# Optimization experiments

Measured on AMD Instinct MI355X. Metric: run time of the kernel, lower is better.

The kernel has to match this reference:

```python
import jax, jax.numpy as jnp
import numpy as np

N, E = 50000, 500000
DH, DL = 13, 128          # handcrafted / learned node feature dims
OH, OL = 32, 96           # node-encoder output dims; node_dim D = OH+OL
D = OH + OL               # 128
EIN = (DH + DL) + 1 + 3 * D + 1  # 527, forced by concat in forward
H = 256                   # MLP hidden width
HC = 64                   # classifier hidden width
EPS = 1e-8


def _mlp(x, W1, b1, W2, b2):
    # 2-layer MLP with ReLU, matching repo MLP(fc_dims=[H, out])
    return jax.nn.relu(x @ W1 + b1) @ W2 + b2


def _cosine(a, b):
    # torch.nn.CosineSimilarity(dim=1, eps=1e-8)
    na = jnp.maximum(jnp.linalg.norm(a, axis=-1), EPS)
    nb = jnp.maximum(jnp.linalg.norm(b, axis=-1), EPS)
    return jnp.sum(a * b, axis=-1) / (na * nb)


def _lin(key, fan_in, fan_out):
    kW, kb = jax.random.split(key)
    s = 1.0 / np.sqrt(fan_in)
    return (jax.random.uniform(kW, (fan_in, fan_out), jnp.float32, -s, s),
            jax.random.uniform(kb, (fan_out,), jnp.float32, -s, s))


def setup_inputs() -> dict:
    key = jax.random.key(0)
    ks = jax.random.split(key, 16)
    x1 = jax.random.normal(ks[0], (N, DH), jnp.float32)
    x2 = jax.random.normal(ks[1], (N, DL), jnp.float32)
    edge_index = jax.random.randint(ks[2], (2, E), 0, N, jnp.int64)
    Wh1, bh1 = _lin(ks[3], DH, H);   Wh2, bh2 = _lin(ks[4], H, OH)
    Wl1, bl1 = _lin(ks[5], DL, H);   Wl2, bl2 = _lin(ks[6], H, OL)
    We1, be1 = _lin(ks[7], EIN, H);  We2, be2 = _lin(ks[8], H, D)
    Wmsg, bmsg = _lin(ks[9], 2 * D, D)
    Wnode, bnode = _lin(ks[10], 2 * D, D)
    Wmp1, bmp1 = _lin(ks[11], 3 * D, H); Wmp2, bmp2 = _lin(ks[12], H, D)
    Wc1, bc1 = _lin(ks[13], D, HC);  Wc2, bc2 = _lin(ks[14], HC, 1)
    return dict(x1=x1, x2=x2, edge_index=edge_index,
                Wh1=Wh1, bh1=bh1, Wh2=Wh2, bh2=bh2,
                Wl1=Wl1, bl1=bl1, Wl2=Wl2, bl2=bl2,
                We1=We1, be1=be1, We2=We2, be2=be2,
                Wmsg=Wmsg, bmsg=bmsg, Wnode=Wnode, bnode=bnode,
                Wmp1=Wmp1, bmp1=bmp1, Wmp2=Wmp2, bmp2=bmp2,
                Wc1=Wc1, bc1=bc1, Wc2=Wc2, bc2=bc2)


def reference(x1, x2, edge_index,
              Wh1, bh1, Wh2, bh2,
              Wl1, bl1, Wl2, bl2,
              We1, be1, We2, be2,
              Wmsg, bmsg, Wnode, bnode,
              Wmp1, bmp1, Wmp2, bmp2,
              Wc1, bc1, Wc2, bc2):
    src, trg = edge_index[0], edge_index[1]
    # raw-feature edge descriptors
    x_init = jnp.concatenate((x1, x2), axis=-1)            # [N, 141]
    xi_s, xi_t = x_init[src], x_init[trg]                  # gathers [E, 141]
    sim1 = _cosine(xi_s, xi_t)                             # [E]
    abs_init = jnp.abs(xi_s - xi_t)                        # [E, 141]
    # node encoders
    h1 = _mlp(x1, Wh1, bh1, Wh2, bh2)                      # [N, 32]
    h2 = _mlp(x2, Wl1, bl1, Wl2, bl2)                      # [N, 96]
    x = jnp.concatenate((h1, h2), axis=-1)                 # [N, 128]
    xs, xt = x[src], x[trg]                                # [E, 128]
    sim2 = _cosine(xs, xt)                                 # [E]
    edge_feat_in = jnp.concatenate(
        (abs_init, sim1[:, None], xs, xt, jnp.abs(xs - xt), sim2[:, None]),
        axis=-1)                                           # [E, 527]
    e = _mlp(edge_feat_in, We1, be1, We2, be2)             # [E, 128]
    # edge MPNN round: edge->node aggregation, node update, edge update
    msg = jax.nn.relu(jnp.concatenate((xs, e), axis=-1) @ Wmsg + bmsg)  # [E, 128]
    agg = jax.ops.segment_sum(msg, trg, num_segments=N)    # [N, 128]
    xn = jax.nn.relu(jnp.concatenate((x, agg), axis=-1) @ Wnode + bnode)  # [N, 128]
    e_mp = _mlp(jnp.concatenate((xn[src], xn[trg], e), axis=-1),
                Wmp1, bmp1, Wmp2, bmp2)                    # [E, 128]
    pred = _mlp(e_mp, Wc1, bc1, Wc2, bc2)                  # [E, 1]
    return jnp.squeeze(pred, axis=-1)                      # [E]
```

## Files before the change

kernel.cpp:

```cpp
#include <hip/hip_runtime.h>
#include <hip/hip_bf16.h>
#include <hip/hip_fp16.h>


using fp16 = __half;
typedef _Float16 h16;
typedef _Float16 f16x8 __attribute__((ext_vector_type(8)));
typedef float f32x4 __attribute__((ext_vector_type(4)));

#define NN 50000
#define EE 500000
#define EPSC 1e-8f

__device__ __forceinline__ float reluf(float v){ return v > 0.f ? v : 0.f; }

#define OFF_E1   0
#define OFF_E2   139264
#define OFF_MSG  172032
#define OFF_NODE 204800
#define OFF_MP1  237568
#define OFF_MP2  335872
#define OFF_C1   368640
#define OFF_N1   376832
#define OFF_N2   458752
#define WT_TOTAL 524288
#define BF_TOTAL 640

__global__ __launch_bounds__(256) void k_prep(
    const float* __restrict__ We1, const float* __restrict__ We2,
    const float* __restrict__ Wmsg, const float* __restrict__ Wnode,
    const float* __restrict__ Wmp1, const float* __restrict__ Wmp2,
    const float* __restrict__ Wc1,
    const float* __restrict__ Wh1, const float* __restrict__ Wl1,
    const float* __restrict__ Wh2, const float* __restrict__ Wl2,
    const float* __restrict__ bh1, const float* __restrict__ bl1,
    const float* __restrict__ bh2, const float* __restrict__ bl2,
    h16* __restrict__ WT, float* __restrict__ BF)
{
  int idx = blockIdx.x * 256 + threadIdx.x;
  if (idx >= WT_TOTAL) {
    const int b = idx - WT_TOTAL;
    if (b < 512) BF[b] = (b < 256) ? bh1[b] : bl1[b - 256];
    else if (b < BF_TOTAL) {
      const int c = b - 512;
      BF[b] = (c < 32) ? bh2[c] : bl2[c - 32];
    }
    return;
  }
  h16 v;
  if (idx < OFF_E2) {
    const int L = idx, n = L / 544, k = L % 544;
    int r;
    if      (k < 128) r = 142 + k;
    else if (k < 256) r = 270 + (k - 128);
    else if (k < 384) r = 398 + (k - 256);
    else if (k < 512) r = 13 + (k - 384);
    else if (k < 525) r = k - 512;
    else if (k == 528) r = 141;
    else if (k == 529) r = 526;
    else r = -1;
    v = (h16)((r >= 0) ? We1[r * 256 + n] : 0.f);
  } else if (idx < OFF_MSG) {
    const int L = idx - OFF_E2, n = L >> 8, k = L & 255;
    v = (h16)We2[k * 128 + n];
  } else if (idx < OFF_NODE) {
    const int L = idx - OFF_MSG, n = L >> 8, k = L & 255;
    const int ko = (k < 128) ? (128 + k) : (k - 128);
    v = (h16)Wmsg[ko * 128 + n];
  } else if (idx < OFF_MP1) {
    const int L = idx - OFF_NODE, n = L >> 8, k = L & 255;
    v = (h16)Wnode[k * 128 + n];
  } else if (idx < OFF_MP2) {
    const int L = idx - OFF_MP1, n = L / 384, k = L % 384;
    v = (h16)Wmp1[k * 256 + n];
  } else if (idx < OFF_C1) {
    const int L = idx - OFF_MP2, n = L >> 8, k = L & 255;
    v = (h16)Wmp2[k * 128 + n];
  } else if (idx < OFF_N1) {
    const int L = idx - OFF_C1, n = L >> 7, k = L & 127;
    v = (h16)Wc1[k * 64 + n];
  } else if (idx < OFF_N2) {
    const int L = idx - OFF_N1, n = L / 160, k = L % 160;
    float f = 0.f;
    if (n < 256) { if (k < 13) f = Wh1[k * 256 + n]; }
    else { if (k >= 16 && k < 144) f = Wl1[(k - 16) * 256 + (n - 256)]; }
    v = (h16)f;
  } else {
    const int L = idx - OFF_N2, n = L >> 9, k = L & 511;
    float f = 0.f;
    if (n < 32) { if (k < 256) f = Wh2[k * 32 + n]; }
    else { if (k >= 256) f = Wl2[(k - 256) * 96 + (n - 32)]; }
    v = (h16)f;
  }
  WT[idx] = v;
}

__global__ __launch_bounds__(256) void k_cvt(
    const float* __restrict__ x1, const float* __restrict__ x2,
    h16* __restrict__ X1P, h16* __restrict__ X2H)
{
  const int idx = blockIdx.x * 256 + threadIdx.x;
  if (idx < NN * 16) {
    const int nn = idx >> 4, j = idx & 15;
    X1P[idx] = (h16)((j < 13) ? x1[nn * 13 + j] : 0.f);
  }
  const int i2 = idx - NN * 16;
  if (i2 >= 0 && i2 < NN * 128) X2H[i2] = (h16)x2[i2];
}

template<int ROWS, int UDIM, int KP, int LDA, int WAVES, bool RELU,
         bool ENDSYNC, typename F>
__device__ __forceinline__ void mfma_gemm(const h16* sA,
    const h16* __restrict__ WT, const float* __restrict__ bias, F emit)
{
  constexpr int RT = ROWS / 16;
  constexpr int NPW0 = UDIM / WAVES;
  constexpr int NPW = (NPW0 < 16) ? 16 : NPW0;
  constexpr int NT = NPW / 16;
  constexpr int NSTEPS = KP / 32;
  constexpr int CH0 = (NT >= 4) ? 2 : 4;
  constexpr int CHUNK = (NSTEPS < CH0) ? NSTEPS : CH0;
  constexpr int NCH = (NSTEPS + CHUNK - 1) / CHUNK;
  const int tid = threadIdx.x;
  const int wave = tid >> 6;
  const int lane = tid & 63;
  const int m = lane & 15;
  const int quad = lane >> 4;
  const int n0 = wave * NPW;
  const bool active = (n0 < UDIM);

  f32x4 acc[RT][NT];
#pragma unroll
  for (int r = 0; r < RT; ++r)
#pragma unroll
    for (int j = 0; j < NT; ++j) acc[r][j] = (f32x4){0.f, 0.f, 0.f, 0.f};
  float bb[NT];

  if (active) {
    const h16* wbase = &WT[(size_t)(n0 + m) * KP + quad * 8];
#pragma unroll
    for (int j = 0; j < NT; ++j) bb[j] = bias[n0 + j * 16 + m];

    f16x8 breg[2][CHUNK][NT];
#pragma unroll
    for (int s = 0; s < CHUNK; ++s)
      if (s < NSTEPS)
#pragma unroll
        for (int j = 0; j < NT; ++j)
          breg[0][s][j] = *(const f16x8*)&wbase[(size_t)j * 16 * KP + s * 32];
    asm volatile("" ::: "memory");

#pragma unroll
    for (int c = 0; c < NCH; ++c) {
      if (c + 1 < NCH) {
#pragma unroll
        for (int s = 0; s < CHUNK; ++s) {
          const int st = (c + 1) * CHUNK + s;
          if (st < NSTEPS)
#pragma unroll
            for (int j = 0; j < NT; ++j)
              breg[(c + 1) & 1][s][j] =
                  *(const f16x8*)&wbase[(size_t)j * 16 * KP + st * 32];
        }
      }
#pragma unroll
      for (int s = 0; s < CHUNK; ++s) {
        const int st = c * CHUNK + s;
        if (st < NSTEPS) {
          const int k0 = st * 32;
#pragma unroll
          for (int r = 0; r < RT; ++r) {
            const f16x8 af = *(const f16x8*)&sA[(r * 16 + m) * LDA + k0 + quad * 8];
#pragma unroll
            for (int j = 0; j < NT; ++j)
              acc[r][j] = __builtin_amdgcn_mfma_f32_16x16x32_f16(af, breg[c & 1][s][j], acc[r][j], 0, 0, 0);
          }
        }
      }
      asm volatile("" ::: "memory");
    }
  }
  __syncthreads();
  if (active) {
#pragma unroll
    for (int j = 0; j < NT; ++j) {
      const int col = n0 + j * 16 + m;
#pragma unroll
      for (int r = 0; r < RT; ++r)
#pragma unroll
        for (int g = 0; g < 4; ++g) {
          const int row = r * 16 + quad * 4 + g;
          float v = acc[r][j][g] + bb[j];
          if (RELU) v = reluf(v);
          emit(row, col, v);
        }
    }
  }
  if (ENDSYNC) __syncthreads();
}

__global__ __launch_bounds__(512, 4) void k_nenc(
    const h16* __restrict__ X1P, const h16* __restrict__ X2H,
    const h16* __restrict__ WT, const float* __restrict__ BF,
    h16* __restrict__ XH)
{
  __shared__ __align__(16) h16 sA[32 * 168];
  __shared__ __align__(16) h16 sH[32 * 520];
  const int tid = threadIdx.x;
  const int n0 = blockIdx.x * 32;
  const int remn = NN - n0;
  const int cnt = remn < 32 ? remn : 32;
  const int n = tid >> 4;
  const int q = tid & 15;

  if (n < cnt) {
    const int node = n0 + n;
    if (q < 2)
      *(f16x8*)&sA[n * 168 + q * 8] = *(const f16x8*)&X1P[node * 16 + q * 8];
    else if (q < 4)
      *(f16x8*)&sA[n * 168 + 144 + (q - 2) * 8] = (f16x8){};
    *(f16x8*)&sA[n * 168 + 16 + q * 8] =
        *(const f16x8*)&X2H[(size_t)node * 128 + q * 8];
  }
  __syncthreads();

  mfma_gemm<32, 512, 160, 168, 8, true, true>(sA, WT + OFF_N1, BF,
      [&](int row, int col, float v) { sH[row * 520 + col] = (h16)v; });
  mfma_gemm<32, 128, 512, 520, 8, false, false>(sH, WT + OFF_N2, BF + 512,
      [&](int row, int col, float v) {
        if (row < cnt) XH[(size_t)(n0 + row) * 128 + col] = (h16)v;
      });
}

__global__ __launch_bounds__(512, 4) void k_edge_mlp(
    const h16* __restrict__ X1P, const h16* __restrict__ X2H,
    const int* __restrict__ ei, const h16* __restrict__ XH,
    const h16* __restrict__ WT,
    const float* __restrict__ be1, const float* __restrict__ be2,
    const float* __restrict__ bmsg,
    h16* __restrict__ EB, float* __restrict__ AGG)
{
  __shared__ __align__(16) h16 sFeat[64 * 568];
  __shared__ int strg[64];
  const int tid = threadIdx.x;
  const long e0 = (long)blockIdx.x * 64;
  const long rem = (long)EE - e0;
  const int cnt = rem < 64 ? (int)rem : 64;
  const int n = tid >> 3;
  const int q = tid & 7;
  h16* Arow = &sFeat[n * 568];
  f16x8 xsv0 = {}, xsv1 = {};

  if (n < cnt) {
    const int s = ei[e0 + n];
    const int t = ei[(long)EE + e0 + n];
    if (q == 0) strg[n] = t;
    float ds = 0.f, ns = 0.f, nt = 0.f;
    if (q < 2) {
      const f16x8 a = *(const f16x8*)&X1P[s * 16 + q * 8];
      const f16x8 b = *(const f16x8*)&X1P[t * 16 + q * 8];
      f16x8 d;
#pragma unroll
      for (int i = 0; i < 8; ++i) {
        const float av = (float)a[i], bv = (float)b[i];
        ds += av * bv; ns += av * av; nt += bv * bv;
        d[i] = (h16)fabsf(av - bv);
      }
      *(f16x8*)&Arow[512 + q * 8] = d;
    }
#pragma unroll
    for (int c = 0; c < 2; ++c) {
      const f16x8 a = *(const f16x8*)&X2H[(size_t)s * 128 + q * 16 + c * 8];
      const f16x8 b = *(const f16x8*)&X2H[(size_t)t * 128 + q * 16 + c * 8];
      f16x8 d;
#pragma unroll
      for (int i = 0; i < 8; ++i) {
        const float av = (float)a[i], bv = (float)b[i];
        ds += av * bv; ns += av * av; nt += bv * bv;
        d[i] = (h16)fabsf(av - bv);
      }
      *(f16x8*)&Arow[384 + q * 16 + c * 8] = d;
    }
    ds += __shfl_xor(ds, 1); ds += __shfl_xor(ds, 2); ds += __shfl_xor(ds, 4);
    ns += __shfl_xor(ns, 1); ns += __shfl_xor(ns, 2); ns += __shfl_xor(ns, 4);
    nt += __shfl_xor(nt, 1); nt += __shfl_xor(nt, 2); nt += __shfl_xor(nt, 4);
    if (q == 0)
      Arow[528] = (h16)(ds / (fmaxf(sqrtf(ns), EPSC) * fmaxf(sqrtf(nt), EPSC)));

    float ds2 = 0.f, ns2 = 0.f, nt2 = 0.f;
#pragma unroll
    for (int c = 0; c < 2; ++c) {
      const f16x8 a = *(const f16x8*)&XH[(size_t)s * 128 + q * 16 + c * 8];
      const f16x8 b = *(const f16x8*)&XH[(size_t)t * 128 + q * 16 + c * 8];
      if (c == 0) xsv0 = a; else xsv1 = a;
      f16x8 d;
#pragma unroll
      for (int i = 0; i < 8; ++i) {
        const float av = (float)a[i], bv = (float)b[i];
        ds2 += av * bv; ns2 += av * av; nt2 += bv * bv;
        d[i] = (h16)fabsf(av - bv);
      }
      *(f16x8*)&Arow[q * 16 + c * 8]       = a;
      *(f16x8*)&Arow[128 + q * 16 + c * 8] = b;
      *(f16x8*)&Arow[256 + q * 16 + c * 8] = d;
    }
    ds2 += __shfl_xor(ds2, 1); ds2 += __shfl_xor(ds2, 2); ds2 += __shfl_xor(ds2, 4);
    ns2 += __shfl_xor(ns2, 1); ns2 += __shfl_xor(ns2, 2); ns2 += __shfl_xor(ns2, 4);
    nt2 += __shfl_xor(nt2, 1); nt2 += __shfl_xor(nt2, 2); nt2 += __shfl_xor(nt2, 4);
    if (q == 0)
      Arow[529] = (h16)(ds2 / (fmaxf(sqrtf(ns2), EPSC) * fmaxf(sqrtf(nt2), EPSC)));
    for (int j = 530 + q; j < 544; j += 8) Arow[j] = (h16)0.f;
  } else {
    if (q == 0) strg[n] = 0;
    for (int j8 = q; j8 < 71; j8 += 8) *(f16x8*)&Arow[j8 * 8] = (f16x8){};
  }
  __syncthreads();

  h16* sHid = sFeat;
  mfma_gemm<64, 256, 544, 568, 8, true, true>(sFeat, WT + OFF_E1, be1,
      [&](int row, int col, float v) { sHid[row * 264 + col] = (h16)v; });
  mfma_gemm<64, 128, 256, 264, 8, false, false>(sHid, WT + OFF_E2, be2,
      [&](int row, int col, float v) {
        const h16 vh = (h16)v;
        if (row < cnt) EB[(size_t)(e0 + row) * 128 + col] = vh;
        sHid[row * 264 + col] = vh;
      });
  *(f16x8*)&sFeat[n * 264 + 128 + q * 16]     = xsv0;
  *(f16x8*)&sFeat[n * 264 + 128 + q * 16 + 8] = xsv1;
  __syncthreads();
  mfma_gemm<64, 128, 256, 264, 8, true, false>(sFeat, WT + OFF_MSG, bmsg,
      [&](int row, int col, float v) {
        if (row < cnt) atomicAdd(&AGG[(size_t)strg[row] * 128 + col], v);
      });
}

__global__ __launch_bounds__(256, 4) void k_node_update(
    const h16* __restrict__ XH, const float* __restrict__ AGG,
    const h16* __restrict__ WT, const float* __restrict__ bnode,
    h16* __restrict__ XNH)
{
  __shared__ __align__(16) h16 sA[64 * 264];
  const int tid = threadIdx.x;
  const int n0 = blockIdx.x * 64;
  const int remn = NN - n0;
  const int cnt = remn < 64 ? remn : 64;
  const int n = tid >> 2;
  const int q = tid & 3;

  if (n < cnt) {
    const f16x8* xr = (const f16x8*)&XH[(size_t)(n0 + n) * 128];
    const float4* ar = (const float4*)&AGG[(size_t)(n0 + n) * 128];
    for (int j8 = q; j8 < 16; j8 += 4)
      *(f16x8*)&sA[n * 264 + j8 * 8] = xr[j8];
    for (int j4 = q; j4 < 32; j4 += 4) {
      const float4 b = ar[j4];
      h16* p1 = &sA[n * 264 + 128 + j4 * 4];
      p1[0] = (h16)b.x; p1[1] = (h16)b.y; p1[2] = (h16)b.z; p1[3] = (h16)b.w;
    }
  } else {
    for (int j = q; j < 256; j += 4) sA[n * 264 + j] = (h16)0.f;
  }
  __syncthreads();

  mfma_gemm<64, 128, 256, 264, 4, true, false>(sA, WT + OFF_NODE, bnode,
      [&](int row, int col, float v) {
        if (row < cnt) XNH[(size_t)(n0 + row) * 128 + col] = (h16)v;
      });
}

__global__ __launch_bounds__(512, 4) void k_empl(
    const int* __restrict__ ei, const h16* __restrict__ XNH,
    const h16* __restrict__ EB, const h16* __restrict__ WT,
    const float* __restrict__ bmp1, const float* __restrict__ bmp2,
    const float* __restrict__ bc1,
    const float* __restrict__ Wc2, const float* __restrict__ bc2,
    float* __restrict__ out)
{
  __shared__ __align__(16) h16 sF[64 * 392];
  const int tid = threadIdx.x;
  const long e0 = (long)blockIdx.x * 64;
  const long rem = (long)EE - e0;
  const int cnt = rem < 64 ? (int)rem : 64;
  const int n = tid >> 3;
  const int q = tid & 7;

  if (n < cnt) {
    const int s = ei[e0 + n];
    const int t = ei[(long)EE + e0 + n];
    const f16x8* xsr = (const f16x8*)&XNH[(size_t)s * 128];
    const f16x8* xtr = (const f16x8*)&XNH[(size_t)t * 128];
    const f16x8* ebr = (const f16x8*)&EB[(size_t)(e0 + n) * 128];
#pragma unroll
    for (int j8 = q; j8 < 16; j8 += 8) {
      *(f16x8*)&sF[n * 392 + j8 * 8]       = xsr[j8];
      *(f16x8*)&sF[n * 392 + 128 + j8 * 8] = xtr[j8];
      *(f16x8*)&sF[n * 392 + 256 + j8 * 8] = ebr[j8];
    }
  } else {
    for (int j8 = q; j8 < 49; j8 += 8) *(f16x8*)&sF[n * 392 + j8 * 8] = (f16x8){};
  }
  __syncthreads();

  h16*  sH2 = sF;
  h16*  sE  = sF;
  float* sHC = (float*)((char*)sF + 17408);
  mfma_gemm<64, 256, 384, 392, 8, true, true>(sF, WT + OFF_MP1, bmp1,
      [&](int row, int col, float v) { sH2[row * 264 + col] = (h16)v; });
  mfma_gemm<64, 128, 256, 264, 8, false, true>(sH2, WT + OFF_MP2, bmp2,
      [&](int row, int col, float v) { sE[row * 136 + col] = (h16)v; });
  mfma_gemm<64, 64, 128, 136, 8, true, true>(sE, WT + OFF_C1, bc1,
      [&](int row, int col, float v) { sHC[row * 65 + col] = v; });
  if (tid < cnt) {
    float acc = bc2[0];
    for (int k = 0; k < 64; ++k) acc += sHC[tid * 65 + k] * Wc2[k];
    out[e0 + tid] = acc;
  }
}

extern "C" void kernel_launch(void* const* d_in, const int* in_sizes, int n_in,
                              void* d_out, int out_size, void* d_ws, size_t ws_size,
                              hipStream_t stream)
{
  const float* x1  = (const float*)d_in[0];
  const float* x2  = (const float*)d_in[1];
  const int*   ei  = (const int*)d_in[2];
  const float* Wh1 = (const float*)d_in[3],  *bh1 = (const float*)d_in[4];
  const float* Wh2 = (const float*)d_in[5],  *bh2 = (const float*)d_in[6];
  const float* Wl1 = (const float*)d_in[7],  *bl1 = (const float*)d_in[8];
  const float* Wl2 = (const float*)d_in[9],  *bl2 = (const float*)d_in[10];
  const float* We1 = (const float*)d_in[11], *be1 = (const float*)d_in[12];
  const float* We2 = (const float*)d_in[13], *be2 = (const float*)d_in[14];
  const float* Wmsg = (const float*)d_in[15], *bmsg = (const float*)d_in[16];
  const float* Wnode = (const float*)d_in[17], *bnode = (const float*)d_in[18];
  const float* Wmp1 = (const float*)d_in[19], *bmp1 = (const float*)d_in[20];
  const float* Wmp2 = (const float*)d_in[21], *bmp2 = (const float*)d_in[22];
  const float* Wc1 = (const float*)d_in[23], *bc1 = (const float*)d_in[24];
  const float* Wc2 = (const float*)d_in[25], *bc2 = (const float*)d_in[26];
  float* out = (float*)d_out;

  float* AGG = (float*)d_ws;
  h16*   EB  = (h16*)(AGG + (size_t)NN * 128);
  h16*   WT  = EB + (size_t)EE * 128;
  h16*   XH  = WT + WT_TOTAL;
  h16*   XNH = XH + (size_t)NN * 128;
  h16*   X1P = XNH + (size_t)NN * 128;
  h16*   X2H = X1P + (size_t)NN * 16;
  float* BF  = (float*)(X2H + (size_t)NN * 128);

  k_prep<<<(WT_TOTAL + BF_TOTAL + 255) / 256, 256, 0, stream>>>(
      We1, We2, Wmsg, Wnode, Wmp1, Wmp2, Wc1,
      Wh1, Wl1, Wh2, Wl2, bh1, bl1, bh2, bl2, WT, BF);
  k_cvt<<<(NN * 16 + NN * 128 + 255) / 256, 256, 0, stream>>>(x1, x2, X1P, X2H);
  hipMemsetAsync(AGG, 0, (size_t)NN * 128 * sizeof(float), stream);
  k_nenc<<<(NN + 31) / 32, 512, 0, stream>>>(X1P, X2H, WT, BF, XH);
  k_edge_mlp<<<7813, 512, 0, stream>>>(X1P, X2H, ei, XH, WT,
                                       be1, be2, bmsg, EB, AGG);
  k_node_update<<<782, 256, 0, stream>>>(XH, AGG, WT, bnode, XNH);
  k_empl<<<7813, 512, 0, stream>>>(ei, XNH, EB, WT, bmp1, bmp2, bc1,
                                   Wc2, bc2, out);
}
```

Before: 858.4 us.

## Sort edges by target and pre-reduce messages in shared memory before atomics

Adds histogram, scan and scatter kernels that counting-sort edges by target node, producing sorted source/target lists and original edge ids. The edge MLP kernel then stages message outputs in shared memory and runs segmented sums over consecutive same-target rows, issuing one atomic per run instead of one per edge. The final kernel writes predictions back through the original edge id. This trades fewer global atomics for extra sort passes, a single-block serial scan, and scattered output writes.

Result: slower. 951.3 us (+10.8%).

```diff
diff --git a/kernel.cpp b/kernel.cpp
--- a/kernel.cpp
+++ b/kernel.cpp
@@ -108,6 +108,54 @@
   if (i2 >= 0 && i2 < NN * 128) X2H[i2] = (h16)x2[i2];
 }
 
+__global__ __launch_bounds__(256) void k_hist(
+    const int* __restrict__ ei, int* __restrict__ CNT)
+{
+  const int e = blockIdx.x * 256 + threadIdx.x;
+  if (e < EE) atomicAdd(&CNT[ei[EE + e]], 1);
+}
+
+__global__ __launch_bounds__(1024) void k_scan(
+    const int* __restrict__ CNT, int* __restrict__ OFF)
+{
+  __shared__ int sdata[1024];
+  __shared__ int scarry;
+  const int tid = threadIdx.x;
+  if (tid == 0) { scarry = 0; OFF[0] = 0; }
+  __syncthreads();
+  for (int base = 0; base < NN; base += 1024) {
+    const int i = base + tid;
+    sdata[tid] = (i < NN) ? CNT[i] : 0;
+    __syncthreads();
+    for (int off = 1; off < 1024; off <<= 1) {
+      const int x = (tid >= off) ? sdata[tid - off] : 0;
+      __syncthreads();
+      sdata[tid] += x;
+      __syncthreads();
+    }
+    const int carry = scarry;
+    if (i < NN) OFF[i + 1] = sdata[tid] + carry;
+    __syncthreads();
+    if (tid == 0) scarry = carry + sdata[1023];
+    __syncthreads();
+  }
+}
+
+__global__ __launch_bounds__(256) void k_scatter(
+    const int* __restrict__ ei, const int* __restrict__ OFF,
+    int* __restrict__ POS, int* __restrict__ ES,
+    int* __restrict__ ET, int* __restrict__ OID)
+{
+  const int e = blockIdx.x * 256 + threadIdx.x;
+  if (e >= EE) return;
+  const int t = ei[EE + e];
+  const int p = atomicAdd(&POS[t], 1);
+  const int idx = OFF[t] + p;
+  ES[idx] = ei[e];
+  ET[idx] = t;
+  OID[idx] = e;
+}
+
 template<int ROWS, int UDIM, int KP, int LDA, int WAVES, bool RELU,
          bool ENDSYNC, typename F>
 __device__ __forceinline__ void mfma_gemm(const h16* sA,
@@ -234,8 +282,8 @@
 
 __global__ __launch_bounds__(512, 4) void k_edge_mlp(
     const h16* __restrict__ X1P, const h16* __restrict__ X2H,
-    const int* __restrict__ ei, const h16* __restrict__ XH,
-    const h16* __restrict__ WT,
+    const int* __restrict__ ES, const int* __restrict__ ET,
+    const h16* __restrict__ XH, const h16* __restrict__ WT,
     const float* __restrict__ be1, const float* __restrict__ be2,
     const float* __restrict__ bmsg,
     h16* __restrict__ EB, float* __restrict__ AGG)
@@ -252,8 +300,8 @@
   f16x8 xsv0 = {}, xsv1 = {};
 
   if (n < cnt) {
-    const int s = ei[e0 + n];
-    const int t = ei[(long)EE + e0 + n];
+    const int s = ES[e0 + n];
+    const int t = ET[e0 + n];
     if (q == 0) strg[n] = t;
     float ds = 0.f, ns = 0.f, nt = 0.f;
     if (q < 2) {
@@ -328,10 +376,29 @@
   *(f16x8*)&sFeat[n * 264 + 128 + q * 16]     = xsv0;
   *(f16x8*)&sFeat[n * 264 + 128 + q * 16 + 8] = xsv1;
   __syncthreads();
-  mfma_gemm<64, 128, 256, 264, 8, true, false>(sFeat, WT + OFF_MSG, bmsg,
+  mfma_gemm<64, 128, 256, 264, 8, true, true>(sFeat, WT + OFF_MSG, bmsg,
       [&](int row, int col, float v) {
-        if (row < cnt) atomicAdd(&AGG[(size_t)strg[row] * 128 + col], v);
+        *(float*)((char*)sFeat + row * 528 + col * 4) = v;
       });
+  {
+    const int c = tid & 127;
+    const int g = tid >> 7;
+    const int r0 = g * 16;
+    if (r0 < cnt) {
+      const int rend = (r0 + 16 < cnt) ? r0 + 16 : cnt;
+      float acc = 0.f;
+      int cur = strg[r0];
+      for (int r = r0; r < rend; ++r) {
+        const int t = strg[r];
+        if (t != cur) {
+          atomicAdd(&AGG[(size_t)cur * 128 + c], acc);
+          acc = 0.f; cur = t;
+        }
+        acc += *(const float*)((const char*)sFeat + r * 528 + c * 4);
+      }
+      atomicAdd(&AGG[(size_t)cur * 128 + c], acc);
+    }
+  }
 }
 
 __global__ __launch_bounds__(256, 4) void k_node_update(
@@ -369,7 +436,8 @@
 }
 
 __global__ __launch_bounds__(512, 4) void k_empl(
-    const int* __restrict__ ei, const h16* __restrict__ XNH,
+    const int* __restrict__ ES, const int* __restrict__ ET,
+    const int* __restrict__ OID, const h16* __restrict__ XNH,
     const h16* __restrict__ EB, const h16* __restrict__ WT,
     const float* __restrict__ bmp1, const float* __restrict__ bmp2,
     const float* __restrict__ bc1,
@@ -385,8 +453,8 @@
   const int q = tid & 7;
 
   if (n < cnt) {
-    const int s = ei[e0 + n];
-    const int t = ei[(long)EE + e0 + n];
+    const int s = ES[e0 + n];
+    const int t = ET[e0 + n];
     const f16x8* xsr = (const f16x8*)&XNH[(size_t)s * 128];
     const f16x8* xtr = (const f16x8*)&XNH[(size_t)t * 128];
     const f16x8* ebr = (const f16x8*)&EB[(size_t)(e0 + n) * 128];
@@ -413,7 +481,7 @@
   if (tid < cnt) {
     float acc = bc2[0];
     for (int k = 0; k < 64; ++k) acc += sHC[tid * 65 + k] * Wc2[k];
-    out[e0 + tid] = acc;
+    out[OID[e0 + tid]] = acc;
   }
 }
 
@@ -446,16 +514,26 @@
   h16*   X1P = XNH + (size_t)NN * 128;
   h16*   X2H = X1P + (size_t)NN * 16;
   float* BF  = (float*)(X2H + (size_t)NN * 128);
+  int*   CNT = (int*)(BF + BF_TOTAL);
+  int*   POS = CNT + NN;
+  int*   OFF = POS + NN;
+  int*   ES  = OFF + (NN + 1);
+  int*   ET  = ES + EE;
+  int*   OID = ET + EE;
 
   k_prep<<<(WT_TOTAL + BF_TOTAL + 255) / 256, 256, 0, stream>>>(
       We1, We2, Wmsg, Wnode, Wmp1, Wmp2, Wc1,
       Wh1, Wl1, Wh2, Wl2, bh1, bl1, bh2, bl2, WT, BF);
   k_cvt<<<(NN * 16 + NN * 128 + 255) / 256, 256, 0, stream>>>(x1, x2, X1P, X2H);
   hipMemsetAsync(AGG, 0, (size_t)NN * 128 * sizeof(float), stream);
+  hipMemsetAsync(CNT, 0, (size_t)2 * NN * sizeof(int), stream);
+  k_hist<<<(EE + 255) / 256, 256, 0, stream>>>(ei, CNT);
+  k_scan<<<1, 1024, 0, stream>>>(CNT, OFF);
+  k_scatter<<<(EE + 255) / 256, 256, 0, stream>>>(ei, OFF, POS, ES, ET, OID);
   k_nenc<<<(NN + 31) / 32, 512, 0, stream>>>(X1P, X2H, WT, BF, XH);
-  k_edge_mlp<<<7813, 512, 0, stream>>>(X1P, X2H, ei, XH, WT,
+  k_edge_mlp<<<7813, 512, 0, stream>>>(X1P, X2H, ES, ET, XH, WT,
                                        be1, be2, bmsg, EB, AGG);
   k_node_update<<<782, 256, 0, stream>>>(XH, AGG, WT, bnode, XNH);
-  k_empl<<<7813, 512, 0, stream>>>(ei, XNH, EB, WT, bmp1, bmp2, bc1,
+  k_empl<<<7813, 512, 0, stream>>>(ES, ET, OID, XNH, EB, WT, bmp1, bmp2, bc1,
                                    Wc2, bc2, out);
 }
```
